# Optimization experiments

Hardware: AMD Instinct MI355X
Metric: run time of the kernel (lower is better)

The kernel has to match this reference:

```python
import jax, jax.numpy as jnp
import numpy as np

N_NODES = 50000
N_EDGES = 800000
N_EVAL = 500000
D = 96


def _sage_conv(x, edge_index, W_l, W_r, b):
    # PyG SAGEConv with aggr='add':
    #   aggr_out[v] = sum_{(u->v) in edges} x[u]
    #   out = aggr_out @ W_l^T-equivalent + b + x @ W_r  (we store W as [in, out])
    src, dst = edge_index[0], edge_index[1]
    msgs = x[src]                                        # [E, d_in] irregular gather
    aggr = jax.ops.segment_sum(msgs, dst, num_segments=x.shape[0])  # [N, d_in]
    return aggr @ W_l + b + x @ W_r                      # [N, d_out]


def setup_inputs() -> dict:
    key = jax.random.key(0)
    ks = jax.random.split(key, 8)
    scale = 1.0 / np.sqrt(D)
    Features = jax.random.normal(ks[0], (N_NODES, D), dtype=jnp.float32)
    A = jax.random.randint(ks[1], (2, N_EDGES), 0, N_NODES, dtype=jnp.int64)
    E = jax.random.randint(ks[2], (2, N_EVAL), 0, N_NODES, dtype=jnp.int64)
    W1_l = jax.random.normal(ks[3], (D, D), dtype=jnp.float32) * scale
    W1_r = jax.random.normal(ks[4], (D, D), dtype=jnp.float32) * scale
    b1 = jnp.zeros((D,), dtype=jnp.float32)
    W2_l = jax.random.normal(ks[5], (D, D), dtype=jnp.float32) * scale
    W2_r = jax.random.normal(ks[6], (D, D), dtype=jnp.float32) * scale
    b2 = jnp.zeros((D,), dtype=jnp.float32)
    return {"Features": Features, "A": A, "E": E,
            "W1_l": W1_l, "W1_r": W1_r, "b1": b1,
            "W2_l": W2_l, "W2_r": W2_r, "b2": b2}


def reference(Features, A, E, W1_l, W1_r, b1, W2_l, W2_r, b2):
    h = _sage_conv(Features, A, W1_l, W1_r, b1)          # [N, hidden]
    h = jax.nn.relu(h)
    # dropout in eval mode = identity
    h = _sage_conv(h, A, W2_l, W2_r, b2)                 # [N, out]
    # edge scoring: gather src/dst embeddings, dot, sigmoid
    src = h[E[0]]                                        # [n_eval, out]
    dst = h[E[1]]                                        # [n_eval, out]
    return jax.nn.sigmoid(jnp.sum(src * dst, axis=-1))   # [n_eval]
```

## Files before the change

### kernel.cpp

```cpp
#include <hip/hip_runtime.h>
#include <math.h>

#define N_NODES 50000
#define N_EDGES 800000
#define N_EVAL  500000
#define CSTRIDE 16
#define MAXDEG  64
#define NB_GEMM ((N_NODES + 63) / 64)
#define NB_AGG  ((N_NODES * 24 + 255) / 256)
#define HALF_EVAL (N_EVAL / 2)

__device__ __forceinline__ float4 f4add(float4 a, float4 b) {
    return make_float4(a.x + b.x, a.y + b.y, a.z + b.z, a.w + b.w);
}
__device__ __forceinline__ float4 f4fma(float s, float4 w, float4 a) {
    return make_float4(fmaf(s, w.x, a.x), fmaf(s, w.y, a.y),
                       fmaf(s, w.z, a.z), fmaf(s, w.w, a.w));
}
__device__ __forceinline__ float4 ld4(const float* p) {
    return *(const float4*)p;
}


__device__ __forceinline__ void bucket_role(int idx, const int* __restrict__ src,
                                            const int* __restrict__ dst,
                                            int* __restrict__ degS,
                                            int* __restrict__ bucket) {
    int t = idx * 256 + threadIdx.x;
    if (t < N_EDGES / 4) {
        int4 s = ((const int4*)src)[t];
        int4 d = ((const int4*)dst)[t];
        int r0 = atomicAdd(&degS[(size_t)d.x * CSTRIDE], 1);
        int r1 = atomicAdd(&degS[(size_t)d.y * CSTRIDE], 1);
        int r2 = atomicAdd(&degS[(size_t)d.z * CSTRIDE], 1);
        int r3 = atomicAdd(&degS[(size_t)d.w * CSTRIDE], 1);
        if (r0 < MAXDEG) bucket[d.x * MAXDEG + r0] = s.x;
        if (r1 < MAXDEG) bucket[d.y * MAXDEG + r1] = s.y;
        if (r2 < MAXDEG) bucket[d.z * MAXDEG + r2] = s.z;
        if (r3 < MAXDEG) bucket[d.w * MAXDEG + r3] = s.w;
    }
}

__device__ __forceinline__ void aggr_role(int idx, const float* __restrict__ x,
                                          const int* __restrict__ degS,
                                          const int* __restrict__ bucket,
                                          float* __restrict__ out) {
    int gt = idx * 256 + threadIdx.x;
    if (gt >= N_NODES * 24) return;
    int v = gt / 24;
    int c = gt - v * 24;
    const float* xp = x + c * 4;
    const int4* bk4 = (const int4*)(bucket + v * MAXDEG);
    int deg = degS[(size_t)v * CSTRIDE];
    int4 q0 = bk4[0], q1 = bk4[1], q2 = bk4[2], q3 = bk4[3];
    int4 q4 = bk4[4], q5 = bk4[5], q6 = bk4[6], q7 = bk4[7];
    if (deg > MAXDEG) deg = MAXDEG;
    const float4 z = make_float4(0.f, 0.f, 0.f, 0.f);
    float4 t0, t1, t2, t3, t4, t5, t6, t7, t8, t9, t10, t11, t12, t13, t14, t15;
    if (deg >= 16) {
        t0  = ld4(xp + (size_t)q0.x * 96);
        t1  = ld4(xp + (size_t)q0.y * 96);
        t2  = ld4(xp + (size_t)q0.z * 96);
        t3  = ld4(xp + (size_t)q0.w * 96);
        t4  = ld4(xp + (size_t)q1.x * 96);
        t5  = ld4(xp + (size_t)q1.y * 96);
        t6  = ld4(xp + (size_t)q1.z * 96);
        t7  = ld4(xp + (size_t)q1.w * 96);
        t8  = ld4(xp + (size_t)q2.x * 96);
        t9  = ld4(xp + (size_t)q2.y * 96);
        t10 = ld4(xp + (size_t)q2.z * 96);
        t11 = ld4(xp + (size_t)q2.w * 96);
        t12 = ld4(xp + (size_t)q3.x * 96);
        t13 = ld4(xp + (size_t)q3.y * 96);
        t14 = ld4(xp + (size_t)q3.z * 96);
        t15 = ld4(xp + (size_t)q3.w * 96);
    } else if (deg >= 8) {
        t0 = ld4(xp + (size_t)q0.x * 96);
        t1 = ld4(xp + (size_t)q0.y * 96);
        t2 = ld4(xp + (size_t)q0.z * 96);
        t3 = ld4(xp + (size_t)q0.w * 96);
        t4 = ld4(xp + (size_t)q1.x * 96);
        t5 = ld4(xp + (size_t)q1.y * 96);
        t6 = ld4(xp + (size_t)q1.z * 96);
        t7 = ld4(xp + (size_t)q1.w * 96);
        t8 = z; t9 = z; t10 = z; t11 = z; t12 = z; t13 = z; t14 = z; t15 = z;
        if (deg > 8)  t8  = ld4(xp + (size_t)q2.x * 96);
        if (deg > 9)  t9  = ld4(xp + (size_t)q2.y * 96);
        if (deg > 10) t10 = ld4(xp + (size_t)q2.z * 96);
        if (deg > 11) t11 = ld4(xp + (size_t)q2.w * 96);
        if (deg > 12) t12 = ld4(xp + (size_t)q3.x * 96);
        if (deg > 13) t13 = ld4(xp + (size_t)q3.y * 96);
        if (deg > 14) t14 = ld4(xp + (size_t)q3.z * 96);
    } else {
        t0 = z; t1 = z; t2 = z; t3 = z; t4 = z; t5 = z; t6 = z; t7 = z;
        t8 = z; t9 = z; t10 = z; t11 = z; t12 = z; t13 = z; t14 = z; t15 = z;
        if (deg > 0) t0 = ld4(xp + (size_t)q0.x * 96);
        if (deg > 1) t1 = ld4(xp + (size_t)q0.y * 96);
        if (deg > 2) t2 = ld4(xp + (size_t)q0.z * 96);
        if (deg > 3) t3 = ld4(xp + (size_t)q0.w * 96);
        if (deg > 4) t4 = ld4(xp + (size_t)q1.x * 96);
        if (deg > 5) t5 = ld4(xp + (size_t)q1.y * 96);
        if (deg > 6) t6 = ld4(xp + (size_t)q1.z * 96);
    }
    float4 a0 = f4add(f4add(f4add(t0, t1), f4add(t2, t3)),
                      f4add(f4add(t4, t5), f4add(t6, t7)));
    float4 a1 = f4add(f4add(f4add(t8, t9), f4add(t10, t11)),
                      f4add(f4add(t12, t13), f4add(t14, t15)));
    if (deg > 16) {
        float4 u0, u1, u2, u3, u4, u5, u6, u7;
        u0 = ld4(xp + (size_t)q4.x * 96);
        u1 = z; u2 = z; u3 = z; u4 = z; u5 = z; u6 = z; u7 = z;
        if (deg > 17) u1 = ld4(xp + (size_t)q4.y * 96);
        if (deg > 18) u2 = ld4(xp + (size_t)q4.z * 96);
        if (deg > 19) u3 = ld4(xp + (size_t)q4.w * 96);
        if (deg > 20) u4 = ld4(xp + (size_t)q5.x * 96);
        if (deg > 21) u5 = ld4(xp + (size_t)q5.y * 96);
        if (deg > 22) u6 = ld4(xp + (size_t)q5.z * 96);
        if (deg > 23) u7 = ld4(xp + (size_t)q5.w * 96);
        a0 = f4add(a0, f4add(f4add(u0, u1), f4add(u2, u3)));
        a1 = f4add(a1, f4add(f4add(u4, u5), f4add(u6, u7)));
    }
    if (deg > 24) {
        float4 u0, u1, u2, u3, u4, u5, u6, u7;
        u0 = ld4(xp + (size_t)q6.x * 96);
        u1 = z; u2 = z; u3 = z; u4 = z; u5 = z; u6 = z; u7 = z;
        if (deg > 25) u1 = ld4(xp + (size_t)q6.y * 96);
        if (deg > 26) u2 = ld4(xp + (size_t)q6.z * 96);
        if (deg > 27) u3 = ld4(xp + (size_t)q6.w * 96);
        if (deg > 28) u4 = ld4(xp + (size_t)q7.x * 96);
        if (deg > 29) u5 = ld4(xp + (size_t)q7.y * 96);
        if (deg > 30) u6 = ld4(xp + (size_t)q7.z * 96);
        if (deg > 31) u7 = ld4(xp + (size_t)q7.w * 96);
        a0 = f4add(a0, f4add(f4add(u0, u1), f4add(u2, u3)));
        a1 = f4add(a1, f4add(f4add(u4, u5), f4add(u6, u7)));
    }
    if (deg > 32) {
        for (int i = 32; i < deg; i += 4) {
            int4 r = bk4[i >> 2];
            float4 s0, s1, s2, s3;
            s0 = ld4(xp + (size_t)r.x * 96);
            s1 = z; s2 = z; s3 = z;
            if (i + 1 < deg) s1 = ld4(xp + (size_t)r.y * 96);
            if (i + 2 < deg) s2 = ld4(xp + (size_t)r.z * 96);
            if (i + 3 < deg) s3 = ld4(xp + (size_t)r.w * 96);
            a0 = f4add(a0, f4add(f4add(s0, s1), f4add(s2, s3)));
        }
    }
    *(float4*)(out + (size_t)v * 96 + c * 4) = f4add(a0, a1);
}

__device__ __forceinline__ void selfgemm_role(int g, const float* __restrict__ X,
                                              const float* __restrict__ W96,
                                              const float* __restrict__ bias,
                                              float* __restrict__ S,
                                              float* __restrict__ Ws,
                                              float* __restrict__ xT) {
    const int tid = threadIdx.x;
    const int j   = tid & 31;
    const int ty  = tid >> 5;
    const int v0  = g * 64;

    float acc[8][3];
    float b0 = bias[j], b1 = bias[j + 32], b2 = bias[j + 64];
    #pragma unroll
    for (int r = 0; r < 8; ++r) { acc[r][0] = b0; acc[r][1] = b1; acc[r][2] = b2; }

    const int sr = tid >> 2;
    const int sc = tid & 3;
    int sv = v0 + sr; if (sv >= N_NODES) sv = N_NODES - 1;

    for (int kc = 0; kc < 3; ++kc) {
        const float* W = W96 + kc * (32 * 96);
        const int kbase = kc * 32;
        __syncthreads();
        #pragma unroll
        for (int i = 0; i < 3; ++i) {
            int f = tid + i * 256;
            *(float4*)(Ws + f * 4) = *(const float4*)(W + f * 4);
        }
        {
            const float* rowp = X + (size_t)sv * 96 + kbase;
            float4 a = *(const float4*)(rowp + sc * 4);
            float4 b = *(const float4*)(rowp + sc * 4 + 16);
            int k0 = sc * 4;
            xT[(k0 + 0) * 68 + sr] = a.x;
            xT[(k0 + 1) * 68 + sr] = a.y;
            xT[(k0 + 2) * 68 + sr] = a.z;
            xT[(k0 + 3) * 68 + sr] = a.w;
            xT[(k0 + 16) * 68 + sr] = b.x;
            xT[(k0 + 17) * 68 + sr] = b.y;
            xT[(k0 + 18) * 68 + sr] = b.z;
            xT[(k0 + 19) * 68 + sr] = b.w;
        }
        __syncthreads();
        #pragma unroll 8
        for (int kk = 0; kk < 32; ++kk) {
            float w0 = Ws[kk * 96 + j];
            float w1 = Ws[kk * 96 + j + 32];
            float w2 = Ws[kk * 96 + j + 64];
            float4 xa = *(const float4*)(xT + kk * 68 + ty * 8);
            float4 xb = *(const float4*)(xT + kk * 68 + ty * 8 + 4);
#define ROWFMA(r, xv)                                   \
            acc[r][0] = fmaf(xv, w0, acc[r][0]);        \
            acc[r][1] = fmaf(xv, w1, acc[r][1]);        \
            acc[r][2] = fmaf(xv, w2, acc[r][2]);
            ROWFMA(0, xa.x) ROWFMA(1, xa.y) ROWFMA(2, xa.z) ROWFMA(3, xa.w)
            ROWFMA(4, xb.x) ROWFMA(5, xb.y) ROWFMA(6, xb.z) ROWFMA(7, xb.w)
#undef ROWFMA
        }
    }
    #pragma unroll
    for (int r = 0; r < 8; ++r) {
        int v = v0 + ty * 8 + r;
        if (v < N_NODES) {
            S[(size_t)v * 96 + j]      = acc[r][0];
            S[(size_t)v * 96 + j + 32] = acc[r][1];
            S[(size_t)v * 96 + j + 64] = acc[r][2];
        }
    }
}


__global__ __launch_bounds__(256) void k_fusedA(const int* __restrict__ src,
                                                const int* __restrict__ dst,
                                                int* __restrict__ degS,
                                                int* __restrict__ bucket,
                                                const float* __restrict__ X,
                                                const float* __restrict__ Wr,
                                                const float* __restrict__ bias,
                                                float* __restrict__ S) {
    __shared__ float Ws[32 * 96];
    __shared__ float xT[32 * 68];
    int b = blockIdx.x;
    if (b & 1) selfgemm_role(b >> 1, X, Wr, bias, S, Ws, xT);
    else       bucket_role(b >> 1, src, dst, degS, bucket);
}

__global__ __launch_bounds__(256, 4) void k_aggr(const float* __restrict__ x,
                                                 const int* __restrict__ degS,
                                                 const int* __restrict__ bucket,
                                                 float* __restrict__ out) {
    aggr_role(blockIdx.x, x, degS, bucket, out);
}

__global__ __launch_bounds__(256, 4) void k_fusedC(const float* __restrict__ h1,
                                                   const int* __restrict__ degS,
                                                   const int* __restrict__ bucket,
                                                   float* __restrict__ aggrOut,
                                                   const float* __restrict__ Wr,
                                                   const float* __restrict__ bias,
                                                   float* __restrict__ S) {
    __shared__ float Ws[32 * 96];
    __shared__ float xT[32 * 68];
    int b = blockIdx.x;
    int g = b / 7, r = b % 7;
    if (r == 3) {
        if (g < NB_GEMM) selfgemm_role(g, h1, Wr, bias, S, Ws, xT);
    } else {
        int idx = g * 6 + (r < 3 ? r : r - 1);
        if (idx < NB_AGG) aggr_role(idx, h1, degS, bucket, aggrOut);
    }
}

template <int RELU>
__global__ __launch_bounds__(192) void k_gemmH(const float* __restrict__ P,
                                               const float* __restrict__ Wl,
                                               const float* __restrict__ S,
                                               float* __restrict__ out) {
    __shared__ float Ws[32 * 96];
    __shared__ float xT[32 * 68];
    const int tid = threadIdx.x;
    const int q   = tid % 24;
    const int rg  = tid / 24;
    const int v0  = blockIdx.x * 64;

    const int  row0 = tid >> 3,         qd0 = tid & 7;
    const int  row1 = (tid + 192) >> 3, qd1 = (tid + 192) & 7;
    const int  row2 = (tid + 384) >> 3, qd2 = (tid + 384) & 7;
    const bool has2 = (tid < 128);
    int sv0 = v0 + row0; if (sv0 >= N_NODES) sv0 = N_NODES - 1;
    int sv1 = v0 + row1; if (sv1 >= N_NODES) sv1 = N_NODES - 1;
    int sv2 = v0 + row2; if (sv2 >= N_NODES) sv2 = N_NODES - 1;

    float4 acc[8];
    #pragma unroll
    for (int r = 0; r < 8; ++r) acc[r] = make_float4(0.f, 0.f, 0.f, 0.f);

    float4 wreg0, wreg1, wreg2, wreg3;
    float4 xreg0, xreg1, xreg2;

    auto load_chunk = [&](int kc) {
        const float* W = Wl + kc * (32 * 96);
        const int kbase = kc * 32;
        wreg0 = *(const float4*)(W + (tid + 0 * 192) * 4);
        wreg1 = *(const float4*)(W + (tid + 1 * 192) * 4);
        wreg2 = *(const float4*)(W + (tid + 2 * 192) * 4);
        wreg3 = *(const float4*)(W + (tid + 3 * 192) * 4);
        xreg0 = *(const float4*)(P + (size_t)sv0 * 96 + kbase + qd0 * 4);
        xreg1 = *(const float4*)(P + (size_t)sv1 * 96 + kbase + qd1 * 4);
        if (has2) xreg2 = *(const float4*)(P + (size_t)sv2 * 96 + kbase + qd2 * 4);
    };
    auto store_chunk = [&]() {
        *(float4*)(Ws + (tid + 0 * 192) * 4) = wreg0;
        *(float4*)(Ws + (tid + 1 * 192) * 4) = wreg1;
        *(float4*)(Ws + (tid + 2 * 192) * 4) = wreg2;
        *(float4*)(Ws + (tid + 3 * 192) * 4) = wreg3;
        int k0 = qd0 * 4;
        xT[(k0 + 0) * 68 + row0] = xreg0.x;
        xT[(k0 + 1) * 68 + row0] = xreg0.y;
        xT[(k0 + 2) * 68 + row0] = xreg0.z;
        xT[(k0 + 3) * 68 + row0] = xreg0.w;
        int k1 = qd1 * 4;
        xT[(k1 + 0) * 68 + row1] = xreg1.x;
        xT[(k1 + 1) * 68 + row1] = xreg1.y;
        xT[(k1 + 2) * 68 + row1] = xreg1.z;
        xT[(k1 + 3) * 68 + row1] = xreg1.w;
        if (has2) {
            int k2 = qd2 * 4;
            xT[(k2 + 0) * 68 + row2] = xreg2.x;
            xT[(k2 + 1) * 68 + row2] = xreg2.y;
            xT[(k2 + 2) * 68 + row2] = xreg2.z;
            xT[(k2 + 3) * 68 + row2] = xreg2.w;
        }
    };

    load_chunk(0);
    for (int kc = 0; kc < 3; ++kc) {
        __syncthreads();
        store_chunk();
        if (kc < 2) load_chunk(kc + 1);
        __syncthreads();
        #pragma unroll 8
        for (int kk = 0; kk < 32; ++kk) {
            float4 w  = *(const float4*)(Ws + kk * 96 + q * 4);
            float4 xa = *(const float4*)(xT + kk * 68 + rg * 8);
            float4 xb = *(const float4*)(xT + kk * 68 + rg * 8 + 4);
            acc[0] = f4fma(xa.x, w, acc[0]);
            acc[1] = f4fma(xa.y, w, acc[1]);
            acc[2] = f4fma(xa.z, w, acc[2]);
            acc[3] = f4fma(xa.w, w, acc[3]);
            acc[4] = f4fma(xb.x, w, acc[4]);
            acc[5] = f4fma(xb.y, w, acc[5]);
            acc[6] = f4fma(xb.z, w, acc[6]);
            acc[7] = f4fma(xb.w, w, acc[7]);
        }
    }
    #pragma unroll
    for (int r = 0; r < 8; ++r) {
        int v = v0 + rg * 8 + r;
        if (v < N_NODES) {
            float4 s4 = *(const float4*)(S + (size_t)v * 96 + q * 4);
            float4 o = f4add(acc[r], s4);
            if (RELU) {
                o.x = fmaxf(o.x, 0.f); o.y = fmaxf(o.y, 0.f);
                o.z = fmaxf(o.z, 0.f); o.w = fmaxf(o.w, 0.f);
            }
            *(float4*)(out + (size_t)v * 96 + q * 4) = o;
        }
    }
}

__global__ __launch_bounds__(256) void k_score(const float* __restrict__ h,
                                               const int* __restrict__ E,
                                               float* __restrict__ out) {
    int t = blockIdx.x * 256 + threadIdx.x;
    int e = t >> 3, sub = t & 7;
    if (e >= HALF_EVAL) return;
    int e2 = e + HALF_EVAL;
    int s0 = E[e];
    int d0 = E[N_EVAL + e];
    int s1 = E[e2];
    int d1 = E[N_EVAL + e2];
    const float* ps0 = h + (size_t)s0 * 96 + sub * 12;
    const float* pd0 = h + (size_t)d0 * 96 + sub * 12;
    const float* ps1 = h + (size_t)s1 * 96 + sub * 12;
    const float* pd1 = h + (size_t)d1 * 96 + sub * 12;
    float4 a0 = ld4(ps0 + 0), a1 = ld4(ps0 + 4), a2 = ld4(ps0 + 8);
    float4 b0 = ld4(pd0 + 0), b1 = ld4(pd0 + 4), b2 = ld4(pd0 + 8);
    float4 c0 = ld4(ps1 + 0), c1 = ld4(ps1 + 4), c2 = ld4(ps1 + 8);
    float4 g0 = ld4(pd1 + 0), g1 = ld4(pd1 + 4), g2 = ld4(pd1 + 8);
    float dot0 = a0.x * b0.x + a0.y * b0.y + a0.z * b0.z + a0.w * b0.w
               + a1.x * b1.x + a1.y * b1.y + a1.z * b1.z + a1.w * b1.w
               + a2.x * b2.x + a2.y * b2.y + a2.z * b2.z + a2.w * b2.w;
    float dot1 = c0.x * g0.x + c0.y * g0.y + c0.z * g0.z + c0.w * g0.w
               + c1.x * g1.x + c1.y * g1.y + c1.z * g1.z + c1.w * g1.w
               + c2.x * g2.x + c2.y * g2.y + c2.z * g2.z + c2.w * g2.w;
    dot0 += __shfl_xor(dot0, 1, 64);
    dot1 += __shfl_xor(dot1, 1, 64);
    dot0 += __shfl_xor(dot0, 2, 64);
    dot1 += __shfl_xor(dot1, 2, 64);
    dot0 += __shfl_xor(dot0, 4, 64);
    dot1 += __shfl_xor(dot1, 4, 64);
    if (sub == 0) {
        out[e]  = 1.f / (1.f + expf(-dot0));
        out[e2] = 1.f / (1.f + expf(-dot1));
    }
}


extern "C" void kernel_launch(void* const* d_in, const int* in_sizes, int n_in,
                              void* d_out, int out_size, void* d_ws, size_t ws_size,
                              hipStream_t stream) {
    const float* Features = (const float*)d_in[0];
    const int*   A        = (const int*)d_in[1];
    const int*   E        = (const int*)d_in[2];
    const float* W1l = (const float*)d_in[3];
    const float* W1r = (const float*)d_in[4];
    const float* b1  = (const float*)d_in[5];
    const float* W2l = (const float*)d_in[6];
    const float* W2r = (const float*)d_in[7];
    const float* b2  = (const float*)d_in[8];
    float* out = (float*)d_out;

    char* p = (char*)d_ws;
    auto alloc = [&](size_t bytes) -> char* {
        char* q = p;
        p += (bytes + 255) & ~(size_t)255;
        return q;
    };
    int*   degS   = (int*)alloc((size_t)N_NODES * CSTRIDE * 4);
    int*   bucket = (int*)alloc((size_t)N_NODES * MAXDEG * 4);
    float* bufA   = (float*)alloc((size_t)N_NODES * 96 * 4);
    float* bufB   = (float*)alloc((size_t)N_NODES * 96 * 4);
    float* bufS   = (float*)alloc((size_t)N_NODES * 96 * 4);

    const int* Asrc = A;
    const int* Adst = A + N_EDGES;

    hipMemsetAsync(degS, 0, (size_t)N_NODES * CSTRIDE * 4, stream);

    k_fusedA<<<2 * NB_GEMM, 256, 0, stream>>>(Asrc, Adst, degS, bucket,
                                              Features, W1r, b1, bufS);
    k_aggr<<<NB_AGG, 256, 0, stream>>>(Features, degS, bucket, bufA);
    k_gemmH<1><<<NB_GEMM, 192, 0, stream>>>(bufA, W1l, bufS, bufB);
    k_fusedC<<<7 * NB_GEMM, 256, 0, stream>>>(bufB, degS, bucket, bufA,
                                              W2r, b2, bufS);
    k_gemmH<0><<<NB_GEMM, 192, 0, stream>>>(bufA, W2l, bufS, bufA);
    k_score<<<(HALF_EVAL * 8 + 255) / 256, 256, 0, stream>>>(bufA, E, out);
}
```

Before: 300.5 us.

## Fuse neighbor aggregation with GEMM into per-layer combo kernels

Replaces the separate aggregation kernel and the register-tiled GEMM kernels with one kernel per layer. Each 384-thread block aggregates 16 nodes into shared memory and then multiplies by W_l, and in layer 2 also by W_r, before writing the output. This removes the round trip of the aggregated features through global memory and two kernel launches. In exchange the GEMM tile is much smaller: each thread holds one float4 accumulator, so weights are reloaded per 16 nodes and there is less register reuse than the previous 64-row tiling.

Measured after the change: 322.7 us. +7.4%, slower.

```diff
diff --git a/kernel.cpp b/kernel.cpp
--- a/kernel.cpp
+++ b/kernel.cpp
@@ -7,7 +7,7 @@
 #define CSTRIDE 16
 #define MAXDEG  64
 #define NB_GEMM ((N_NODES + 63) / 64)
-#define NB_AGG  ((N_NODES * 24 + 255) / 256)
+#define NB_COMBO (N_NODES / 16)
 #define HALF_EVAL (N_EVAL / 2)
 
 __device__ __forceinline__ float4 f4add(float4 a, float4 b) {
@@ -41,14 +41,10 @@
     }
 }
 
-__device__ __forceinline__ void aggr_role(int idx, const float* __restrict__ x,
-                                          const int* __restrict__ degS,
-                                          const int* __restrict__ bucket,
-                                          float* __restrict__ out) {
-    int gt = idx * 256 + threadIdx.x;
-    if (gt >= N_NODES * 24) return;
-    int v = gt / 24;
-    int c = gt - v * 24;
+__device__ __forceinline__ float4 aggr_compute(int v, int c,
+                                               const float* __restrict__ x,
+                                               const int* __restrict__ degS,
+                                               const int* __restrict__ bucket) {
     const float* xp = x + c * 4;
     const int4* bk4 = (const int4*)(bucket + v * MAXDEG);
     int deg = degS[(size_t)v * CSTRIDE];
@@ -146,7 +142,7 @@
             a0 = f4add(a0, f4add(f4add(s0, s1), f4add(s2, s3)));
         }
     }
-    *(float4*)(out + (size_t)v * 96 + c * 4) = f4add(a0, a1);
+    return f4add(a0, a1);
 }
 
 __device__ __forceinline__ void selfgemm_role(int g, const float* __restrict__ X,
@@ -236,128 +232,70 @@
     else       bucket_role(b >> 1, src, dst, degS, bucket);
 }
 
-__global__ __launch_bounds__(256, 4) void k_aggr(const float* __restrict__ x,
-                                                 const int* __restrict__ degS,
-                                                 const int* __restrict__ bucket,
-                                                 float* __restrict__ out) {
-    aggr_role(blockIdx.x, x, degS, bucket, out);
-}
-
-__global__ __launch_bounds__(256, 4) void k_fusedC(const float* __restrict__ h1,
-                                                   const int* __restrict__ degS,
-                                                   const int* __restrict__ bucket,
-                                                   float* __restrict__ aggrOut,
-                                                   const float* __restrict__ Wr,
-                                                   const float* __restrict__ bias,
-                                                   float* __restrict__ S) {
+template <int L2>
+__global__ __launch_bounds__(384, 2) void k_combo(const float* __restrict__ x,
+                                                  const int* __restrict__ degS,
+                                                  const int* __restrict__ bucket,
+                                                  const float* __restrict__ Wl,
+                                                  const float* __restrict__ Wr,
+                                                  const float* __restrict__ Sb,
+                                                  float* __restrict__ out) {
+    __shared__ float xTa[96 * 17];
+    __shared__ float xTl[L2 ? 96 * 17 : 1];
     __shared__ float Ws[32 * 96];
-    __shared__ float xT[32 * 68];
-    int b = blockIdx.x;
-    int g = b / 7, r = b % 7;
-    if (r == 3) {
-        if (g < NB_GEMM) selfgemm_role(g, h1, Wr, bias, S, Ws, xT);
+
+    const int tid = threadIdx.x;
+    const int v0  = blockIdx.x * 16;
+    const int r   = tid / 24;
+    const int jq  = tid - r * 24;
+
+    {
+        float4 res = aggr_compute(v0 + r, jq, x, degS, bucket);
+        int k0 = jq * 4;
+        xTa[(k0 + 0) * 17 + r] = res.x;
+        xTa[(k0 + 1) * 17 + r] = res.y;
+        xTa[(k0 + 2) * 17 + r] = res.z;
+        xTa[(k0 + 3) * 17 + r] = res.w;
+    }
+
+    float4 acc;
+    if (L2) {
+        acc = ld4(Sb + jq * 4);
+        float4 h = ld4(x + (size_t)(v0 + r) * 96 + jq * 4);
+        int k0 = jq * 4;
+        xTl[(k0 + 0) * 17 + r] = h.x;
+        xTl[(k0 + 1) * 17 + r] = h.y;
+        xTl[(k0 + 2) * 17 + r] = h.z;
+        xTl[(k0 + 3) * 17 + r] = h.w;
     } else {
-        int idx = g * 6 + (r < 3 ? r : r - 1);
-        if (idx < NB_AGG) aggr_role(idx, h1, degS, bucket, aggrOut);
-    }
-}
-
-template <int RELU>
-__global__ __launch_bounds__(192) void k_gemmH(const float* __restrict__ P,
-                                               const float* __restrict__ Wl,
-                                               const float* __restrict__ S,
-                                               float* __restrict__ out) {
-    __shared__ float Ws[32 * 96];
-    __shared__ float xT[32 * 68];
-    const int tid = threadIdx.x;
-    const int q   = tid % 24;
-    const int rg  = tid / 24;
-    const int v0  = blockIdx.x * 64;
-
-    const int  row0 = tid >> 3,         qd0 = tid & 7;
-    const int  row1 = (tid + 192) >> 3, qd1 = (tid + 192) & 7;
-    const int  row2 = (tid + 384) >> 3, qd2 = (tid + 384) & 7;
-    const bool has2 = (tid < 128);
-    int sv0 = v0 + row0; if (sv0 >= N_NODES) sv0 = N_NODES - 1;
-    int sv1 = v0 + row1; if (sv1 >= N_NODES) sv1 = N_NODES - 1;
-    int sv2 = v0 + row2; if (sv2 >= N_NODES) sv2 = N_NODES - 1;
-
-    float4 acc[8];
-    #pragma unroll
-    for (int r = 0; r < 8; ++r) acc[r] = make_float4(0.f, 0.f, 0.f, 0.f);
-
-    float4 wreg0, wreg1, wreg2, wreg3;
-    float4 xreg0, xreg1, xreg2;
-
-    auto load_chunk = [&](int kc) {
-        const float* W = Wl + kc * (32 * 96);
-        const int kbase = kc * 32;
-        wreg0 = *(const float4*)(W + (tid + 0 * 192) * 4);
-        wreg1 = *(const float4*)(W + (tid + 1 * 192) * 4);
-        wreg2 = *(const float4*)(W + (tid + 2 * 192) * 4);
-        wreg3 = *(const float4*)(W + (tid + 3 * 192) * 4);
-        xreg0 = *(const float4*)(P + (size_t)sv0 * 96 + kbase + qd0 * 4);
-        xreg1 = *(const float4*)(P + (size_t)sv1 * 96 + kbase + qd1 * 4);
-        if (has2) xreg2 = *(const float4*)(P + (size_t)sv2 * 96 + kbase + qd2 * 4);
-    };
-    auto store_chunk = [&]() {
-        *(float4*)(Ws + (tid + 0 * 192) * 4) = wreg0;
-        *(float4*)(Ws + (tid + 1 * 192) * 4) = wreg1;
-        *(float4*)(Ws + (tid + 2 * 192) * 4) = wreg2;
-        *(float4*)(Ws + (tid + 3 * 192) * 4) = wreg3;
-        int k0 = qd0 * 4;
-        xT[(k0 + 0) * 68 + row0] = xreg0.x;
-        xT[(k0 + 1) * 68 + row0] = xreg0.y;
-        xT[(k0 + 2) * 68 + row0] = xreg0.z;
-        xT[(k0 + 3) * 68 + row0] = xreg0.w;
-        int k1 = qd1 * 4;
-        xT[(k1 + 0) * 68 + row1] = xreg1.x;
-        xT[(k1 + 1) * 68 + row1] = xreg1.y;
-        xT[(k1 + 2) * 68 + row1] = xreg1.z;
-        xT[(k1 + 3) * 68 + row1] = xreg1.w;
-        if (has2) {
-            int k2 = qd2 * 4;
-            xT[(k2 + 0) * 68 + row2] = xreg2.x;
-            xT[(k2 + 1) * 68 + row2] = xreg2.y;
-            xT[(k2 + 2) * 68 + row2] = xreg2.z;
-            xT[(k2 + 3) * 68 + row2] = xreg2.w;
-        }
-    };
-
-    load_chunk(0);
-    for (int kc = 0; kc < 3; ++kc) {
+        acc = ld4(Sb + (size_t)(v0 + r) * 96 + jq * 4);
+    }
+
+    const int NCH = L2 ? 6 : 3;
+    for (int cc = 0; cc < NCH; ++cc) {
+        const int kc = (cc >= 3) ? cc - 3 : cc;
+        const float* W = (L2 && cc >= 3) ? (Wr + kc * (32 * 96))
+                                         : (Wl + kc * (32 * 96));
+        const float* xT = (L2 && cc >= 3) ? xTl : xTa;
         __syncthreads();
-        store_chunk();
-        if (kc < 2) load_chunk(kc + 1);
+        #pragma unroll
+        for (int i = 0; i < 2; ++i) {
+            int f = tid + i * 384;
+            *(float4*)(Ws + f * 4) = ld4(W + f * 4);
+        }
         __syncthreads();
         #pragma unroll 8
         for (int kk = 0; kk < 32; ++kk) {
-            float4 w  = *(const float4*)(Ws + kk * 96 + q * 4);
-            float4 xa = *(const float4*)(xT + kk * 68 + rg * 8);
-            float4 xb = *(const float4*)(xT + kk * 68 + rg * 8 + 4);
-            acc[0] = f4fma(xa.x, w, acc[0]);
-            acc[1] = f4fma(xa.y, w, acc[1]);
-            acc[2] = f4fma(xa.z, w, acc[2]);
-            acc[3] = f4fma(xa.w, w, acc[3]);
-            acc[4] = f4fma(xb.x, w, acc[4]);
-            acc[5] = f4fma(xb.y, w, acc[5]);
-            acc[6] = f4fma(xb.z, w, acc[6]);
-            acc[7] = f4fma(xb.w, w, acc[7]);
-        }
-    }
-    #pragma unroll
-    for (int r = 0; r < 8; ++r) {
-        int v = v0 + rg * 8 + r;
-        if (v < N_NODES) {
-            float4 s4 = *(const float4*)(S + (size_t)v * 96 + q * 4);
-            float4 o = f4add(acc[r], s4);
-            if (RELU) {
-                o.x = fmaxf(o.x, 0.f); o.y = fmaxf(o.y, 0.f);
-                o.z = fmaxf(o.z, 0.f); o.w = fmaxf(o.w, 0.f);
-            }
-            *(float4*)(out + (size_t)v * 96 + q * 4) = o;
-        }
-    }
+            float  xv = xT[(kc * 32 + kk) * 17 + r];
+            float4 w  = ld4(Ws + kk * 96 + jq * 4);
+            acc = f4fma(xv, w, acc);
+        }
+    }
+    if (!L2) {
+        acc.x = fmaxf(acc.x, 0.f); acc.y = fmaxf(acc.y, 0.f);
+        acc.z = fmaxf(acc.z, 0.f); acc.w = fmaxf(acc.w, 0.f);
+    }
+    *(float4*)(out + (size_t)(v0 + r) * 96 + jq * 4) = acc;
 }
 
 __global__ __launch_bounds__(256) void k_score(const float* __restrict__ h,
@@ -431,10 +369,9 @@
 
     k_fusedA<<<2 * NB_GEMM, 256, 0, stream>>>(Asrc, Adst, degS, bucket,
                                               Features, W1r, b1, bufS);
-    k_aggr<<<NB_AGG, 256, 0, stream>>>(Features, degS, bucket, bufA);
-    k_gemmH<1><<<NB_GEMM, 192, 0, stream>>>(bufA, W1l, bufS, bufB);
-    k_fusedC<<<7 * NB_GEMM, 256, 0, stream>>>(bufB, degS, bucket, bufA,
-                                              W2r, b2, bufS);
-    k_gemmH<0><<<NB_GEMM, 192, 0, stream>>>(bufA, W2l, bufS, bufA);
+    k_combo<0><<<NB_COMBO, 384, 0, stream>>>(Features, degS, bucket,
+                                             W1l, W1r, bufS, bufB);
+    k_combo<1><<<NB_COMBO, 384, 0, stream>>>(bufB, degS, bucket,
+                                             W2l, W2r, b2, bufA);
     k_score<<<(HALF_EVAL * 8 + 255) / 256, 256, 0, stream>>>(bufA, E, out);
 }
```

## Use 16-bit neighbor buckets and XCC-aware sliced dynamic work queues for aggregation

Applied to the files above, without the earlier changes.

Stores neighbor indices as unsigned short, which halves bucket footprint, and compacts the strided degree array into a dense capped array in a new small kernel. Aggregation is reorganized so each block handles one 16-column feature slice for 64 nodes. Blocks take work from per-slice atomic queues, starting at their XCC id, so each XCD's L2 tends to hold one slice of the feature matrix. This adds a kernel launch, atomic work grabbing and a block barrier, and it relies on node ids fitting in 16 bits (true for 50000 nodes).

Measured after the change: 420.0 us. 39.8% more time.

```diff
diff --git a/kernel.cpp b/kernel.cpp
--- a/kernel.cpp
+++ b/kernel.cpp
@@ -7,7 +7,8 @@
 #define CSTRIDE 16
 #define MAXDEG  64
 #define NB_GEMM ((N_NODES + 63) / 64)
-#define NB_AGG  ((N_NODES * 24 + 255) / 256)
+#define RPQ     ((N_NODES + 63) / 64)
+#define NSLICE  6
 #define HALF_EVAL (N_EVAL / 2)
 
 __device__ __forceinline__ float4 f4add(float4 a, float4 b) {
@@ -25,7 +26,7 @@
 __device__ __forceinline__ void bucket_role(int idx, const int* __restrict__ src,
                                             const int* __restrict__ dst,
                                             int* __restrict__ degS,
-                                            int* __restrict__ bucket) {
+                                            unsigned short* __restrict__ bucket) {
     int t = idx * 256 + threadIdx.x;
     if (t < N_EDGES / 4) {
         int4 s = ((const int4*)src)[t];
@@ -34,73 +35,84 @@
         int r1 = atomicAdd(&degS[(size_t)d.y * CSTRIDE], 1);
         int r2 = atomicAdd(&degS[(size_t)d.z * CSTRIDE], 1);
         int r3 = atomicAdd(&degS[(size_t)d.w * CSTRIDE], 1);
-        if (r0 < MAXDEG) bucket[d.x * MAXDEG + r0] = s.x;
-        if (r1 < MAXDEG) bucket[d.y * MAXDEG + r1] = s.y;
-        if (r2 < MAXDEG) bucket[d.z * MAXDEG + r2] = s.z;
-        if (r3 < MAXDEG) bucket[d.w * MAXDEG + r3] = s.w;
-    }
-}
-
-__device__ __forceinline__ void aggr_role(int idx, const float* __restrict__ x,
-                                          const int* __restrict__ degS,
-                                          const int* __restrict__ bucket,
-                                          float* __restrict__ out) {
-    int gt = idx * 256 + threadIdx.x;
-    if (gt >= N_NODES * 24) return;
-    int v = gt / 24;
-    int c = gt - v * 24;
+        if (r0 < MAXDEG) bucket[(size_t)d.x * MAXDEG + r0] = (unsigned short)s.x;
+        if (r1 < MAXDEG) bucket[(size_t)d.y * MAXDEG + r1] = (unsigned short)s.y;
+        if (r2 < MAXDEG) bucket[(size_t)d.z * MAXDEG + r2] = (unsigned short)s.z;
+        if (r3 < MAXDEG) bucket[(size_t)d.w * MAXDEG + r3] = (unsigned short)s.w;
+    }
+}
+
+__device__ __forceinline__ float4 aggr_compute16(int v, int c,
+        const float* __restrict__ x, const int* __restrict__ degC,
+        const unsigned short* __restrict__ bucket) {
     const float* xp = x + c * 4;
-    const int4* bk4 = (const int4*)(bucket + v * MAXDEG);
-    int deg = degS[(size_t)v * CSTRIDE];
-    int4 q0 = bk4[0], q1 = bk4[1], q2 = bk4[2], q3 = bk4[3];
-    int4 q4 = bk4[4], q5 = bk4[5], q6 = bk4[6], q7 = bk4[7];
-    if (deg > MAXDEG) deg = MAXDEG;
+    const int4* bk4 = (const int4*)(bucket + (size_t)v * MAXDEG);
+    int deg = degC[v];
+    int4 p0 = bk4[0], p1 = bk4[1], p2 = bk4[2], p3 = bk4[3];
+    int idx[32];
+    idx[0]  = p0.x & 0xffff; idx[1]  = (int)((unsigned)p0.x >> 16);
+    idx[2]  = p0.y & 0xffff; idx[3]  = (int)((unsigned)p0.y >> 16);
+    idx[4]  = p0.z & 0xffff; idx[5]  = (int)((unsigned)p0.z >> 16);
+    idx[6]  = p0.w & 0xffff; idx[7]  = (int)((unsigned)p0.w >> 16);
+    idx[8]  = p1.x & 0xffff; idx[9]  = (int)((unsigned)p1.x >> 16);
+    idx[10] = p1.y & 0xffff; idx[11] = (int)((unsigned)p1.y >> 16);
+    idx[12] = p1.z & 0xffff; idx[13] = (int)((unsigned)p1.z >> 16);
+    idx[14] = p1.w & 0xffff; idx[15] = (int)((unsigned)p1.w >> 16);
+    idx[16] = p2.x & 0xffff; idx[17] = (int)((unsigned)p2.x >> 16);
+    idx[18] = p2.y & 0xffff; idx[19] = (int)((unsigned)p2.y >> 16);
+    idx[20] = p2.z & 0xffff; idx[21] = (int)((unsigned)p2.z >> 16);
+    idx[22] = p2.w & 0xffff; idx[23] = (int)((unsigned)p2.w >> 16);
+    idx[24] = p3.x & 0xffff; idx[25] = (int)((unsigned)p3.x >> 16);
+    idx[26] = p3.y & 0xffff; idx[27] = (int)((unsigned)p3.y >> 16);
+    idx[28] = p3.z & 0xffff; idx[29] = (int)((unsigned)p3.z >> 16);
+    idx[30] = p3.w & 0xffff; idx[31] = (int)((unsigned)p3.w >> 16);
+
     const float4 z = make_float4(0.f, 0.f, 0.f, 0.f);
     float4 t0, t1, t2, t3, t4, t5, t6, t7, t8, t9, t10, t11, t12, t13, t14, t15;
     if (deg >= 16) {
-        t0  = ld4(xp + (size_t)q0.x * 96);
-        t1  = ld4(xp + (size_t)q0.y * 96);
-        t2  = ld4(xp + (size_t)q0.z * 96);
-        t3  = ld4(xp + (size_t)q0.w * 96);
-        t4  = ld4(xp + (size_t)q1.x * 96);
-        t5  = ld4(xp + (size_t)q1.y * 96);
-        t6  = ld4(xp + (size_t)q1.z * 96);
-        t7  = ld4(xp + (size_t)q1.w * 96);
-        t8  = ld4(xp + (size_t)q2.x * 96);
-        t9  = ld4(xp + (size_t)q2.y * 96);
-        t10 = ld4(xp + (size_t)q2.z * 96);
-        t11 = ld4(xp + (size_t)q2.w * 96);
-        t12 = ld4(xp + (size_t)q3.x * 96);
-        t13 = ld4(xp + (size_t)q3.y * 96);
-        t14 = ld4(xp + (size_t)q3.z * 96);
-        t15 = ld4(xp + (size_t)q3.w * 96);
+        t0  = ld4(xp + (size_t)idx[0]  * 96);
+        t1  = ld4(xp + (size_t)idx[1]  * 96);
+        t2  = ld4(xp + (size_t)idx[2]  * 96);
+        t3  = ld4(xp + (size_t)idx[3]  * 96);
+        t4  = ld4(xp + (size_t)idx[4]  * 96);
+        t5  = ld4(xp + (size_t)idx[5]  * 96);
+        t6  = ld4(xp + (size_t)idx[6]  * 96);
+        t7  = ld4(xp + (size_t)idx[7]  * 96);
+        t8  = ld4(xp + (size_t)idx[8]  * 96);
+        t9  = ld4(xp + (size_t)idx[9]  * 96);
+        t10 = ld4(xp + (size_t)idx[10] * 96);
+        t11 = ld4(xp + (size_t)idx[11] * 96);
+        t12 = ld4(xp + (size_t)idx[12] * 96);
+        t13 = ld4(xp + (size_t)idx[13] * 96);
+        t14 = ld4(xp + (size_t)idx[14] * 96);
+        t15 = ld4(xp + (size_t)idx[15] * 96);
     } else if (deg >= 8) {
-        t0 = ld4(xp + (size_t)q0.x * 96);
-        t1 = ld4(xp + (size_t)q0.y * 96);
-        t2 = ld4(xp + (size_t)q0.z * 96);
-        t3 = ld4(xp + (size_t)q0.w * 96);
-        t4 = ld4(xp + (size_t)q1.x * 96);
-        t5 = ld4(xp + (size_t)q1.y * 96);
-        t6 = ld4(xp + (size_t)q1.z * 96);
-        t7 = ld4(xp + (size_t)q1.w * 96);
+        t0 = ld4(xp + (size_t)idx[0] * 96);
+        t1 = ld4(xp + (size_t)idx[1] * 96);
+        t2 = ld4(xp + (size_t)idx[2] * 96);
+        t3 = ld4(xp + (size_t)idx[3] * 96);
+        t4 = ld4(xp + (size_t)idx[4] * 96);
+        t5 = ld4(xp + (size_t)idx[5] * 96);
+        t6 = ld4(xp + (size_t)idx[6] * 96);
+        t7 = ld4(xp + (size_t)idx[7] * 96);
         t8 = z; t9 = z; t10 = z; t11 = z; t12 = z; t13 = z; t14 = z; t15 = z;
-        if (deg > 8)  t8  = ld4(xp + (size_t)q2.x * 96);
-        if (deg > 9)  t9  = ld4(xp + (size_t)q2.y * 96);
-        if (deg > 10) t10 = ld4(xp + (size_t)q2.z * 96);
-        if (deg > 11) t11 = ld4(xp + (size_t)q2.w * 96);
-        if (deg > 12) t12 = ld4(xp + (size_t)q3.x * 96);
-        if (deg > 13) t13 = ld4(xp + (size_t)q3.y * 96);
-        if (deg > 14) t14 = ld4(xp + (size_t)q3.z * 96);
+        if (deg > 8)  t8  = ld4(xp + (size_t)idx[8]  * 96);
+        if (deg > 9)  t9  = ld4(xp + (size_t)idx[9]  * 96);
+        if (deg > 10) t10 = ld4(xp + (size_t)idx[10] * 96);
+        if (deg > 11) t11 = ld4(xp + (size_t)idx[11] * 96);
+        if (deg > 12) t12 = ld4(xp + (size_t)idx[12] * 96);
+        if (deg > 13) t13 = ld4(xp + (size_t)idx[13] * 96);
+        if (deg > 14) t14 = ld4(xp + (size_t)idx[14] * 96);
     } else {
         t0 = z; t1 = z; t2 = z; t3 = z; t4 = z; t5 = z; t6 = z; t7 = z;
         t8 = z; t9 = z; t10 = z; t11 = z; t12 = z; t13 = z; t14 = z; t15 = z;
-        if (deg > 0) t0 = ld4(xp + (size_t)q0.x * 96);
-        if (deg > 1) t1 = ld4(xp + (size_t)q0.y * 96);
-        if (deg > 2) t2 = ld4(xp + (size_t)q0.z * 96);
-        if (deg > 3) t3 = ld4(xp + (size_t)q0.w * 96);
-        if (deg > 4) t4 = ld4(xp + (size_t)q1.x * 96);
-        if (deg > 5) t5 = ld4(xp + (size_t)q1.y * 96);
-        if (deg > 6) t6 = ld4(xp + (size_t)q1.z * 96);
+        if (deg > 0) t0 = ld4(xp + (size_t)idx[0] * 96);
+        if (deg > 1) t1 = ld4(xp + (size_t)idx[1] * 96);
+        if (deg > 2) t2 = ld4(xp + (size_t)idx[2] * 96);
+        if (deg > 3) t3 = ld4(xp + (size_t)idx[3] * 96);
+        if (deg > 4) t4 = ld4(xp + (size_t)idx[4] * 96);
+        if (deg > 5) t5 = ld4(xp + (size_t)idx[5] * 96);
+        if (deg > 6) t6 = ld4(xp + (size_t)idx[6] * 96);
     }
     float4 a0 = f4add(f4add(f4add(t0, t1), f4add(t2, t3)),
                       f4add(f4add(t4, t5), f4add(t6, t7)));
@@ -108,45 +120,68 @@
                       f4add(f4add(t12, t13), f4add(t14, t15)));
     if (deg > 16) {
         float4 u0, u1, u2, u3, u4, u5, u6, u7;
-        u0 = ld4(xp + (size_t)q4.x * 96);
+        u0 = ld4(xp + (size_t)idx[16] * 96);
         u1 = z; u2 = z; u3 = z; u4 = z; u5 = z; u6 = z; u7 = z;
-        if (deg > 17) u1 = ld4(xp + (size_t)q4.y * 96);
-        if (deg > 18) u2 = ld4(xp + (size_t)q4.z * 96);
-        if (deg > 19) u3 = ld4(xp + (size_t)q4.w * 96);
-        if (deg > 20) u4 = ld4(xp + (size_t)q5.x * 96);
-        if (deg > 21) u5 = ld4(xp + (size_t)q5.y * 96);
-        if (deg > 22) u6 = ld4(xp + (size_t)q5.z * 96);
-        if (deg > 23) u7 = ld4(xp + (size_t)q5.w * 96);
+        if (deg > 17) u1 = ld4(xp + (size_t)idx[17] * 96);
+        if (deg > 18) u2 = ld4(xp + (size_t)idx[18] * 96);
+        if (deg > 19) u3 = ld4(xp + (size_t)idx[19] * 96);
+        if (deg > 20) u4 = ld4(xp + (size_t)idx[20] * 96);
+        if (deg > 21) u5 = ld4(xp + (size_t)idx[21] * 96);
+        if (deg > 22) u6 = ld4(xp + (size_t)idx[22] * 96);
+        if (deg > 23) u7 = ld4(xp + (size_t)idx[23] * 96);
         a0 = f4add(a0, f4add(f4add(u0, u1), f4add(u2, u3)));
         a1 = f4add(a1, f4add(f4add(u4, u5), f4add(u6, u7)));
     }
     if (deg > 24) {
         float4 u0, u1, u2, u3, u4, u5, u6, u7;
-        u0 = ld4(xp + (size_t)q6.x * 96);
+        u0 = ld4(xp + (size_t)idx[24] * 96);
         u1 = z; u2 = z; u3 = z; u4 = z; u5 = z; u6 = z; u7 = z;
-        if (deg > 25) u1 = ld4(xp + (size_t)q6.y * 96);
-        if (deg > 26) u2 = ld4(xp + (size_t)q6.z * 96);
-        if (deg > 27) u3 = ld4(xp + (size_t)q6.w * 96);
-        if (deg > 28) u4 = ld4(xp + (size_t)q7.x * 96);
-        if (deg > 29) u5 = ld4(xp + (size_t)q7.y * 96);
-        if (deg > 30) u6 = ld4(xp + (size_t)q7.z * 96);
-        if (deg > 31) u7 = ld4(xp + (size_t)q7.w * 96);
+        if (deg > 25) u1 = ld4(xp + (size_t)idx[25] * 96);
+        if (deg > 26) u2 = ld4(xp + (size_t)idx[26] * 96);
+        if (deg > 27) u3 = ld4(xp + (size_t)idx[27] * 96);
+        if (deg > 28) u4 = ld4(xp + (size_t)idx[28] * 96);
+        if (deg > 29) u5 = ld4(xp + (size_t)idx[29] * 96);
+        if (deg > 30) u6 = ld4(xp + (size_t)idx[30] * 96);
+        if (deg > 31) u7 = ld4(xp + (size_t)idx[31] * 96);
         a0 = f4add(a0, f4add(f4add(u0, u1), f4add(u2, u3)));
         a1 = f4add(a1, f4add(f4add(u4, u5), f4add(u6, u7)));
     }
     if (deg > 32) {
-        for (int i = 32; i < deg; i += 4) {
-            int4 r = bk4[i >> 2];
-            float4 s0, s1, s2, s3;
-            s0 = ld4(xp + (size_t)r.x * 96);
-            s1 = z; s2 = z; s3 = z;
-            if (i + 1 < deg) s1 = ld4(xp + (size_t)r.y * 96);
-            if (i + 2 < deg) s2 = ld4(xp + (size_t)r.z * 96);
-            if (i + 3 < deg) s3 = ld4(xp + (size_t)r.w * 96);
-            a0 = f4add(a0, f4add(f4add(s0, s1), f4add(s2, s3)));
-        }
-    }
-    *(float4*)(out + (size_t)v * 96 + c * 4) = f4add(a0, a1);
+        const unsigned short* bk = bucket + (size_t)v * MAXDEG;
+        for (int i = 32; i < deg; ++i)
+            a0 = f4add(a0, ld4(xp + (size_t)bk[i] * 96));
+    }
+    return f4add(a0, a1);
+}
+
+__device__ __forceinline__ int2 grab_work(int* __restrict__ qctr) {
+    __shared__ int s_sl, s_rg;
+    if (threadIdx.x == 0) {
+        unsigned xcc;
+        asm volatile("s_getreg_b32 %0, hwreg(HW_REG_XCC_ID)" : "=s"(xcc));
+        int start = (int)(xcc & 7);
+        if (start >= NSLICE) start -= NSLICE;
+        int sl = -1, rg = -1;
+        for (int k = 0; k < NSLICE; ++k) {
+            int s = start + k; if (s >= NSLICE) s -= NSLICE;
+            int i = atomicAdd(&qctr[s], 1);
+            if (i < RPQ) { sl = s; rg = i; break; }
+        }
+        s_sl = sl; s_rg = rg;
+    }
+    __syncthreads();
+    return make_int2(s_sl, s_rg);
+}
+
+__device__ __forceinline__ void aggrS_role(int slice, int range,
+        const float* __restrict__ x, const int* __restrict__ degC,
+        const unsigned short* __restrict__ bucket, float* __restrict__ out) {
+    int t = threadIdx.x;
+    int v = range * 64 + (t >> 2);
+    if (v >= N_NODES) return;
+    int c = slice * 4 + (t & 3);
+    float4 res = aggr_compute16(v, c, x, degC, bucket);
+    *(float4*)(out + (size_t)v * 96 + c * 4) = res;
 }
 
 __device__ __forceinline__ void selfgemm_role(int g, const float* __restrict__ X,
@@ -224,7 +259,7 @@
 __global__ __launch_bounds__(256) void k_fusedA(const int* __restrict__ src,
                                                 const int* __restrict__ dst,
                                                 int* __restrict__ degS,
-                                                int* __restrict__ bucket,
+                                                unsigned short* __restrict__ bucket,
                                                 const float* __restrict__ X,
                                                 const float* __restrict__ Wr,
                                                 const float* __restrict__ bias,
@@ -236,30 +271,43 @@
     else       bucket_role(b >> 1, src, dst, degS, bucket);
 }
 
-__global__ __launch_bounds__(256, 4) void k_aggr(const float* __restrict__ x,
-                                                 const int* __restrict__ degS,
-                                                 const int* __restrict__ bucket,
-                                                 float* __restrict__ out) {
-    aggr_role(blockIdx.x, x, degS, bucket, out);
-}
-
-__global__ __launch_bounds__(256, 4) void k_fusedC(const float* __restrict__ h1,
-                                                   const int* __restrict__ degS,
-                                                   const int* __restrict__ bucket,
-                                                   float* __restrict__ aggrOut,
-                                                   const float* __restrict__ Wr,
-                                                   const float* __restrict__ bias,
-                                                   float* __restrict__ S) {
+__global__ __launch_bounds__(256) void k_compact(const int* __restrict__ degS,
+                                                 int* __restrict__ degC) {
+    int v = blockIdx.x * 256 + threadIdx.x;
+    if (v < N_NODES) {
+        int d = degS[(size_t)v * CSTRIDE];
+        degC[v] = d > MAXDEG ? MAXDEG : d;
+    }
+}
+
+__global__ __launch_bounds__(256, 4) void k_aggrS(const float* __restrict__ x,
+                                                  const int* __restrict__ degC,
+                                                  const unsigned short* __restrict__ bucket,
+                                                  int* __restrict__ qctr,
+                                                  float* __restrict__ out) {
+    int2 w = grab_work(qctr);
+    if (w.x < 0) return;
+    aggrS_role(w.x, w.y, x, degC, bucket, out);
+}
+
+__global__ __launch_bounds__(256, 4) void k_fusedC2(const float* __restrict__ h1,
+                                                    const int* __restrict__ degC,
+                                                    const unsigned short* __restrict__ bucket,
+                                                    int* __restrict__ qctr,
+                                                    float* __restrict__ aggrOut,
+                                                    const float* __restrict__ Wr,
+                                                    const float* __restrict__ bias,
+                                                    float* __restrict__ S) {
     __shared__ float Ws[32 * 96];
     __shared__ float xT[32 * 68];
     int b = blockIdx.x;
-    int g = b / 7, r = b % 7;
-    if (r == 3) {
-        if (g < NB_GEMM) selfgemm_role(g, h1, Wr, bias, S, Ws, xT);
-    } else {
-        int idx = g * 6 + (r < 3 ? r : r - 1);
-        if (idx < NB_AGG) aggr_role(idx, h1, degS, bucket, aggrOut);
-    }
+    if (b % 7 == 3) {
+        selfgemm_role(b / 7, h1, Wr, bias, S, Ws, xT);
+        return;
+    }
+    int2 w = grab_work(qctr);
+    if (w.x < 0) return;
+    aggrS_role(w.x, w.y, h1, degC, bucket, aggrOut);
 }
 
 template <int RELU>
@@ -419,7 +467,10 @@
         return q;
     };
     int*   degS   = (int*)alloc((size_t)N_NODES * CSTRIDE * 4);
-    int*   bucket = (int*)alloc((size_t)N_NODES * MAXDEG * 4);
+    int*   degC   = (int*)alloc((size_t)N_NODES * 4);
+    unsigned short* bucket =
+        (unsigned short*)alloc((size_t)N_NODES * MAXDEG * 2);
+    int*   qctr   = (int*)alloc(256);
     float* bufA   = (float*)alloc((size_t)N_NODES * 96 * 4);
     float* bufB   = (float*)alloc((size_t)N_NODES * 96 * 4);
     float* bufS   = (float*)alloc((size_t)N_NODES * 96 * 4);
@@ -428,13 +479,15 @@
     const int* Adst = A + N_EDGES;
 
     hipMemsetAsync(degS, 0, (size_t)N_NODES * CSTRIDE * 4, stream);
+    hipMemsetAsync(qctr, 0, 256, stream);
 
     k_fusedA<<<2 * NB_GEMM, 256, 0, stream>>>(Asrc, Adst, degS, bucket,
                                               Features, W1r, b1, bufS);
-    k_aggr<<<NB_AGG, 256, 0, stream>>>(Features, degS, bucket, bufA);
+    k_compact<<<(N_NODES + 255) / 256, 256, 0, stream>>>(degS, degC);
+    k_aggrS<<<NSLICE * RPQ, 256, 0, stream>>>(Features, degC, bucket, qctr, bufA);
     k_gemmH<1><<<NB_GEMM, 192, 0, stream>>>(bufA, W1l, bufS, bufB);
-    k_fusedC<<<7 * NB_GEMM, 256, 0, stream>>>(bufB, degS, bucket, bufA,
-                                              W2r, b2, bufS);
+    k_fusedC2<<<7 * RPQ, 256, 0, stream>>>(bufB, degC, bucket, qctr + 8,
+                                           bufA, W2r, b2, bufS);
     k_gemmH<0><<<NB_GEMM, 192, 0, stream>>>(bufA, W2l, bufS, bufA);
     k_score<<<(HALF_EVAL * 8 + 255) / 256, 256, 0, stream>>>(bufA, E, out);
 }
```
